# Kernel tuning notes

Measured on AMD Instinct MI355X. Metric: run time of the kernel, lower is better.

The kernel has to match this reference:

```python
import jax, jax.numpy as jnp
import numpy as np
from jax import lax

NCLASSES = 3
NMS_PRE = 100
NMS_THR = 0.01
SCORE_THR = 0.1
MAX_NUM = 50
H, W = 248, 216
BS = 16


def make_anchors():
    # Faithful to Anchors(ranges, sizes, rotations) in __init__.
    z0s = np.array([-0.6, -0.6, -1.78], np.float32)
    sizes = np.array([[0.6, 0.8, 1.73], [0.6, 1.76, 1.73], [1.6, 3.9, 1.56]], np.float32)
    rotations = np.array([0.0, 1.57], np.float32)
    x = (np.arange(W, dtype=np.float32) + 0.5) * (69.12 / W)
    y = (np.arange(H, dtype=np.float32) + 0.5) * (79.36 / H) - 39.68
    yy, xx = np.meshgrid(y, x, indexing='ij')  # (H, W)
    anchors = np.zeros((H, W, 3, 2, 7), np.float32)
    for c in range(3):
        for r in range(2):
            anchors[:, :, c, r, 0] = xx
            anchors[:, :, c, r, 1] = yy
            anchors[:, :, c, r, 2] = z0s[c]
            anchors[:, :, c, r, 3:6] = sizes[c]
            anchors[:, :, c, r, 6] = rotations[r]
    return jnp.asarray(anchors)


def setup_inputs() -> dict:
    key = jax.random.key(0)
    k1, k2, k3 = jax.random.split(key, 3)
    return {
        'bbox_cls_pred': jax.random.normal(k1, (BS, 18, H, W), jnp.float32),
        'bbox_pred': jax.random.normal(k2, (BS, 42, H, W), jnp.float32) * 0.1,
        'bbox_dir_cls_pred': jax.random.normal(k3, (BS, 12, H, W), jnp.float32),
        'anchors': make_anchors(),
    }


def limit_period(val, offset=1.0, period=np.pi):
    return val - jnp.floor(val / period + offset) * period


def anchors2bboxes(anchors, deltas):
    xa, ya, za, wa, la, ha, ra = [anchors[:, i] for i in range(7)]
    dx, dy, dz, dw, dl, dh, dr = [deltas[:, i] for i in range(7)]
    da = jnp.sqrt(wa * wa + la * la)
    x = dx * da + xa
    y = dy * da + ya
    z = dz * ha + za + ha * 0.5
    w = wa * jnp.exp(dw)
    l = la * jnp.exp(dl)
    h = ha * jnp.exp(dh)
    z = z - h * 0.5
    theta = ra + dr
    return jnp.stack([x, y, z, w, l, h, theta], axis=-1)


def nms_keep(boxes2d, scores, valid, thresh):
    # Greedy NMS over fixed NMS_PRE boxes; invalid boxes never kept / never suppress.
    n = scores.shape[0]
    order = jnp.argsort(-jnp.where(valid, scores, -jnp.inf))
    b = boxes2d[order]
    v = valid[order]
    area = (b[:, 2] - b[:, 0]) * (b[:, 3] - b[:, 1])
    x1 = jnp.maximum(b[:, None, 0], b[None, :, 0])
    y1 = jnp.maximum(b[:, None, 1], b[None, :, 1])
    x2 = jnp.minimum(b[:, None, 2], b[None, :, 2])
    y2 = jnp.minimum(b[:, None, 3], b[None, :, 3])
    inter = jnp.maximum(x2 - x1, 0.0) * jnp.maximum(y2 - y1, 0.0)
    iou = inter / (area[:, None] + area[None, :] - inter + 1e-8)
    idx = jnp.arange(n)
    def body(i, keep):
        sup = (iou[i] > thresh) & (idx > i) & keep[i]
        return keep & ~sup
    keep = lax.fori_loop(0, n, body, v)
    return jnp.zeros(n, bool).at[order].set(keep)


def process_single(cls_pred, box_pred, dir_pred, anchors):
    # cls_pred (18,H,W), box_pred (42,H,W), dir_pred (12,H,W), anchors (H,W,3,2,7)
    cls = jnp.transpose(cls_pred, (1, 2, 0)).reshape(-1, NCLASSES)
    box = jnp.transpose(box_pred, (1, 2, 0)).reshape(-1, 7)
    dirp = jnp.transpose(dir_pred, (1, 2, 0)).reshape(-1, 2)
    anc = anchors.reshape(-1, 7)
    cls = jax.nn.sigmoid(cls)
    dir_cls = jnp.argmax(dirp, axis=1)
    _, inds = lax.top_k(jnp.max(cls, axis=1), NMS_PRE)
    cls = cls[inds]
    box = box[inds]
    dir_cls = dir_cls[inds]
    anc = anc[inds]
    bboxes = anchors2bboxes(anc, box)  # (NMS_PRE, 7): x,y,z,w,l,h,theta
    xy = bboxes[:, :2]
    wl = bboxes[:, 3:5]
    boxes2d = jnp.concatenate([xy - wl / 2, xy + wl / 2], axis=-1)
    # Torch code detaches theta through limit_period; dir term is constant.
    theta = lax.stop_gradient(limit_period(bboxes[:, 6])) + (1.0 - dir_cls.astype(bboxes.dtype)) * np.pi
    bboxes = bboxes.at[:, 6].set(theta)
    keeps = []
    for c in range(NCLASSES):
        sc = cls[:, c]
        valid = sc > SCORE_THR
        keeps.append(nms_keep(boxes2d, sc, valid, NMS_THR) & valid)
    keep = jnp.stack(keeps)            # (3, NMS_PRE)
    scores_all = cls.T                 # (3, NMS_PRE)
    flat = jnp.where(keep, scores_all, -1.0).reshape(-1)
    final_scores, fi = lax.top_k(flat, MAX_NUM)
    sel = fi % NMS_PRE
    labels = fi // NMS_PRE
    out_bboxes = bboxes[sel]
    mask = final_scores > 0.0
    return out_bboxes, labels, final_scores, mask


def reference(bbox_cls_pred, bbox_pred, bbox_dir_cls_pred, anchors):
    f = jax.vmap(process_single, in_axes=(0, 0, 0, None))
    return f(bbox_cls_pred, bbox_pred, bbox_dir_cls_pred, anchors)
```

## Files before the change

### kernel.cpp

```cpp
#include <hip/hip_runtime.h>
#include <cstdint>

#pragma clang fp contract(off)

#define HH 248
#define WW 216
#define HW (HH*WW)
#define NROW (6*HW)
#define BATCH 16
#define NPRE 100
#define MAXNUM 50
#define NB 2048
#define CAP 2048
#define SBLK 53
#define K0 64
#define NSLOT (SBLK*K0)
#define QMAX 14
#define PIF 3.14159274101257324f

#define T0BKT 1966u

#define CNTB_OFF 0
#define KEYS_OFF 3584
#define SH_OFF   (KEYS_OFF + BATCH*SBLK*K0*8)

__device__ __forceinline__ float sigmoidf_ref(float x) {
    if (x >= 0.0f) {
        return 1.0f / (1.0f + expf(-x));
    } else {
        float e = expf(x);
        return e / (1.0f + e);
    }
}

__device__ __forceinline__ unsigned bucket_of(unsigned bits) {
    unsigned b = (bits >= 0x3F000000u) ? (1024u + ((bits - 0x3F000000u) >> 13))
                                       : (bits >> 20);
    return (b > (unsigned)(NB - 1)) ? (unsigned)(NB - 1) : b;
}

__device__ __forceinline__ void emit_one(unsigned bits, unsigned row,
                                         unsigned* hist, unsigned* lcnt,
                                         unsigned long long* kseg) {
    unsigned bk = bucket_of(bits);
    atomicAdd(&hist[bk], 1u);
    if (bk >= T0BKT) {
        unsigned pos = atomicAdd(lcnt, 1u);
        if (pos < (unsigned)K0)
            kseg[pos] = ((unsigned long long)bits << 32) |
                        (unsigned long long)(0xFFFFFFFFu - row);
    }
}

__global__ __launch_bounds__(256) void k_score(const float* __restrict__ cls,
                                               unsigned short* __restrict__ subhist,
                                               unsigned* __restrict__ cntB,
                                               unsigned long long* __restrict__ keys) {
    int t = threadIdx.x, blk = blockIdx.x, b = blockIdx.y;
    __shared__ unsigned hist[NB];
    __shared__ unsigned lcnt;
    for (int i = t; i < NB; i += 256) hist[i] = 0;
    if (t == 0) lcnt = 0;
    __syncthreads();

    unsigned long long* kseg = keys + (size_t)(b * SBLK + blk) * K0;
    int cell0 = blk * 1024 + t * 4;
    if (cell0 < HW) {
        const float* p = cls + (size_t)b * 18 * HW;
        #pragma unroll
        for (int a = 0; a < 6; ++a) {
            float4 l0 = *(const float4*)(p + (size_t)(a*3+0)*HW + cell0);
            float4 l1 = *(const float4*)(p + (size_t)(a*3+1)*HW + cell0);
            float4 l2 = *(const float4*)(p + (size_t)(a*3+2)*HW + cell0);
            unsigned b0 = __float_as_uint(sigmoidf_ref(fmaxf(l0.x, fmaxf(l1.x, l2.x))));
            unsigned b1 = __float_as_uint(sigmoidf_ref(fmaxf(l0.y, fmaxf(l1.y, l2.y))));
            unsigned b2 = __float_as_uint(sigmoidf_ref(fmaxf(l0.z, fmaxf(l1.z, l2.z))));
            unsigned b3 = __float_as_uint(sigmoidf_ref(fmaxf(l0.w, fmaxf(l1.w, l2.w))));
            emit_one(b0, (unsigned)((cell0+0)*6 + a), hist, &lcnt, kseg);
            emit_one(b1, (unsigned)((cell0+1)*6 + a), hist, &lcnt, kseg);
            emit_one(b2, (unsigned)((cell0+2)*6 + a), hist, &lcnt, kseg);
            emit_one(b3, (unsigned)((cell0+3)*6 + a), hist, &lcnt, kseg);
        }
    }
    __syncthreads();
    unsigned short* sh = subhist + (size_t)(b * SBLK + blk) * NB;
    for (int i = t; i < NB; i += 256) sh[i] = (unsigned short)hist[i];
    if (t == 0) cntB[b * SBLK + blk] = lcnt;
}

__global__ __launch_bounds__(256) void k_final(
    const float* __restrict__ cls, const float* __restrict__ box,
    const float* __restrict__ dir, const float* __restrict__ anc,
    const unsigned* __restrict__ cntB, const unsigned long long* __restrict__ keys,
    const unsigned short* __restrict__ subhist,
    float* __restrict__ out) {
    int b = blockIdx.x, t = threadIdx.x;

    __shared__ unsigned long long keyS[CAP];
    __shared__ int   selRow[NPRE];
    __shared__ float bb[NPRE][7];
    __shared__ float b2d[NPRE][4];
    __shared__ float areaS[NPRE];
    __shared__ float clsS[3][NPRE];
    __shared__ float svalS[3][NPRE];
    __shared__ int   ordS[3][NPRE];
    __shared__ int   rankS[3][NPRE];
    __shared__ float4 sbox[3][NPRE];
    __shared__ float  sarea[3][NPRE];
    __shared__ unsigned keepInit[3][4];
    __shared__ unsigned long long maskS[3][NPRE][2];
    __shared__ unsigned long long keepBits[3][2];
    __shared__ float flatS[3*NPRE];
    __shared__ unsigned hq[256];
    __shared__ unsigned wq[4];
    __shared__ unsigned cntS[SBLK];
    __shared__ int  tbS;
    __shared__ unsigned StbS;
    __shared__ int  safeS;
    __shared__ unsigned mcnt;

    if (t == 0) { tbS = -1; StbS = 0; mcnt = 0; }
    if (t < SBLK) cntS[t] = cntB[b * SBLK + t];
    __syncthreads();

    unsigned long long kq[QMAX];
    #pragma unroll
    for (int q = 0; q < QMAX; ++q) {
        unsigned long long kk = 0ULL;
        int s = t + q * 256;
        if (s < NSLOT) {
            int k = s >> 6, i = s & 63;
            if ((unsigned)i < cntS[k])
                kk = keys[(size_t)(b * SBLK + k) * K0 + i];
        }
        kq[q] = kk;
    }

    {
        const unsigned short* base = subhist + (size_t)b * SBLK * NB;
        unsigned carry = 0;
        for (int c0 = NB - 256; c0 >= 0; c0 -= 256) {
            unsigned s = 0;
            #pragma unroll 4
            for (int k = 0; k < SBLK; ++k) s += base[(size_t)k * NB + (c0 + t)];
            unsigned val = s;
            int lane = t & 63;
            #pragma unroll
            for (int d = 1; d < 64; d <<= 1) {
                unsigned y = __shfl_down(val, d, 64);
                if (lane + d < 64) val += y;
            }
            if (lane == 0) wq[t >> 6] = val;
            __syncthreads();
            unsigned tail = 0;
            for (int w2 = (t >> 6) + 1; w2 < 4; ++w2) tail += wq[w2];
            unsigned S = val + tail + carry;
            hq[t] = S;
            __syncthreads();
            unsigned Snext = (t < 255) ? hq[t + 1] : carry;
            if (S >= (unsigned)NPRE && Snext < (unsigned)NPRE) {
                tbS = c0 + t;
                StbS = S;
            }
            __syncthreads();
            if (tbS >= 0) break;
            carry = hq[0];
        }
    }
    int tb = (tbS < 0) ? 0 : tbS;

    if (t < 64) {
        unsigned c = (t < SBLK) ? cntS[t] : 0u;
        unsigned long long ov = __ballot(c > (unsigned)K0);
        if (t == 0)
            safeS = (tbS >= (int)T0BKT) && (ov == 0ULL) &&
                    (StbS <= (unsigned)CAP) ? 1 : 0;
    }
    __syncthreads();

    int M;
    if (safeS) {
        #pragma unroll
        for (int q = 0; q < QMAX; ++q) {
            unsigned long long kk = kq[q];
            if (bucket_of((unsigned)(kk >> 32)) >= (unsigned)tb) {
                unsigned pos = atomicAdd(&mcnt, 1u);
                keyS[pos] = kk;
            }
        }
        __syncthreads();
        M = (int)mcnt;
    } else {
        const float* p = cls + (size_t)b * 18 * HW;
        for (int cell = t; cell < HW; cell += 256) {
            for (int a = 0; a < 6; ++a) {
                float v0 = p[(size_t)(a*3+0)*HW + cell];
                float v1 = p[(size_t)(a*3+1)*HW + cell];
                float v2 = p[(size_t)(a*3+2)*HW + cell];
                unsigned bits = __float_as_uint(sigmoidf_ref(fmaxf(v0, fmaxf(v1, v2))));
                if (bucket_of(bits) >= (unsigned)tb) {
                    unsigned pos = atomicAdd(&mcnt, 1u);
                    if (pos < (unsigned)CAP)
                        keyS[pos] = ((unsigned long long)bits << 32) |
                                    (unsigned long long)(0xFFFFFFFFu - (unsigned)(cell*6 + a));
                }
            }
        }
        __syncthreads();
        M = (mcnt < (unsigned)CAP) ? (int)mcnt : CAP;
    }
    __syncthreads();

    for (int i = t; i < M; i += 256) {
        unsigned long long k = keyS[i];
        int r = 0;
        int j = 0;
        for (; j + 3 < M; j += 4) {
            unsigned long long a0 = keyS[j+0], a1 = keyS[j+1];
            unsigned long long a2 = keyS[j+2], a3 = keyS[j+3];
            r += (int)(a0 > k) + (int)(a1 > k) + (int)(a2 > k) + (int)(a3 > k);
        }
        for (; j < M; ++j) r += (int)(keyS[j] > k);
        if (r < NPRE) selRow[r] = (int)(0xFFFFFFFFu - (unsigned)(k & 0xFFFFFFFFull));
    }
    __syncthreads();

    if (t < NPRE) {
        int row = selRow[t];
        int a = row % 6;
        int cell = row / 6;
        const float* cb = cls + (size_t)b * 18 * HW + cell;
        clsS[0][t] = sigmoidf_ref(cb[(size_t)(a*3+0)*HW]);
        clsS[1][t] = sigmoidf_ref(cb[(size_t)(a*3+1)*HW]);
        clsS[2][t] = sigmoidf_ref(cb[(size_t)(a*3+2)*HW]);
        const float* db = dir + (size_t)b * 12 * HW + cell;
        float d0 = db[(size_t)(a*2+0)*HW];
        float d1 = db[(size_t)(a*2+1)*HW];
        int dircls = (d1 > d0) ? 1 : 0;
        const float* pb = box + (size_t)b * 42 * HW + cell;
        float dx = pb[(size_t)(a*7+0)*HW], dy = pb[(size_t)(a*7+1)*HW], dz = pb[(size_t)(a*7+2)*HW];
        float dw = pb[(size_t)(a*7+3)*HW], dl = pb[(size_t)(a*7+4)*HW], dh = pb[(size_t)(a*7+5)*HW];
        float dr = pb[(size_t)(a*7+6)*HW];
        const float* ab = anc + (size_t)row * 7;
        float xa = ab[0], ya = ab[1], za = ab[2];
        float wa = ab[3], la = ab[4], ha = ab[5], ra = ab[6];
        float da = sqrtf(wa*wa + la*la);
        float x = dx*da + xa;
        float y = dy*da + ya;
        float z = dz*ha + za + ha*0.5f;
        float wv = wa*expf(dw);
        float lv = la*expf(dl);
        float hv = ha*expf(dh);
        z = z - hv*0.5f;
        float th0 = ra + dr;
        float lim = th0 - floorf(th0/PIF + 1.0f)*PIF;
        float theta = lim + (1.0f - (float)dircls)*PIF;
        bb[t][0]=x; bb[t][1]=y; bb[t][2]=z; bb[t][3]=wv; bb[t][4]=lv; bb[t][5]=hv; bb[t][6]=theta;
        b2d[t][0] = x - wv*0.5f;
        b2d[t][1] = y - lv*0.5f;
        b2d[t][2] = x + wv*0.5f;
        b2d[t][3] = y + lv*0.5f;
        areaS[t] = (b2d[t][2]-b2d[t][0]) * (b2d[t][3]-b2d[t][1]);
    }
    if (t < 12) keepInit[t/4][t%4] = 0u;
    __syncthreads();

    for (int w = t; w < 3*NPRE; w += 256) {
        int c = w / NPRE, p = w % NPRE;
        float sc = clsS[c][p];
        svalS[c][p] = (sc > 0.1f) ? sc : -INFINITY;
    }
    __syncthreads();

    for (int w = t; w < 3*NPRE; w += 256) {
        int c = w / NPRE, p = w % NPRE;
        float v = svalS[c][p];
        int r = 0;
        for (int j0 = 0; j0 < NPRE; j0 += 4) {
            float v0 = svalS[c][j0+0], v1 = svalS[c][j0+1];
            float v2 = svalS[c][j0+2], v3 = svalS[c][j0+3];
            r += (int)(v0 > v || (v0 == v && (j0+0) < p));
            r += (int)(v1 > v || (v1 == v && (j0+1) < p));
            r += (int)(v2 > v || (v2 == v && (j0+2) < p));
            r += (int)(v3 > v || (v3 == v && (j0+3) < p));
        }
        ordS[c][r] = p;
        rankS[c][p] = r;
        if (v != -INFINITY) atomicOr(&keepInit[c][r >> 5], 1u << (r & 31));
    }
    __syncthreads();

    for (int w = t; w < 3*NPRE; w += 256) {
        int c = w / NPRE, i = w % NPRE;
        int pi = ordS[c][i];
        sbox[c][i] = make_float4(b2d[pi][0], b2d[pi][1], b2d[pi][2], b2d[pi][3]);
        sarea[c][i] = areaS[pi];
    }
    __syncthreads();

    for (int w = t; w < 3*NPRE; w += 256) {
        int c = w / NPRE, i = w % NPRE;
        float4 bi = sbox[c][i];
        float ai = sarea[c][i];
        unsigned long long m0 = 0ULL, m1 = 0ULL;
        #pragma unroll 2
        for (int j = i + 1; j < NPRE; ++j) {
            float4 bj = sbox[c][j];
            float x1 = fmaxf(bi.x, bj.x);
            float y1 = fmaxf(bi.y, bj.y);
            float x2 = fminf(bi.z, bj.z);
            float y2 = fminf(bi.w, bj.w);
            float inter = fmaxf(x2 - x1, 0.0f) * fmaxf(y2 - y1, 0.0f);
            float iou = inter / (ai + sarea[c][j] - inter + 1e-8f);
            unsigned long long hit = (iou > 0.01f) ? 1ULL : 0ULL;
            if (j < 64) m0 |= hit << j;
            else        m1 |= hit << (j - 64);
        }
        maskS[c][i][0] = m0;
        maskS[c][i][1] = m1;
    }
    __syncthreads();

    if (t < 3) {
        int c = t;
        unsigned long long k0 = (unsigned long long)keepInit[c][0] |
                                ((unsigned long long)keepInit[c][1] << 32);
        unsigned long long k1 = (unsigned long long)keepInit[c][2] |
                                ((unsigned long long)keepInit[c][3] << 32);
        unsigned long long todo = k0;
        while (todo) {
            int i = __builtin_ctzll(todo);
            unsigned long long m0 = maskS[c][i][0];
            unsigned long long m1 = maskS[c][i][1];
            k0 &= ~m0;
            k1 &= ~m1;
            todo = (todo & (todo - 1)) & ~m0;
        }
        todo = k1;
        while (todo) {
            int i = __builtin_ctzll(todo);
            unsigned long long m1 = maskS[c][64 + i][1];
            k1 &= ~m1;
            todo = (todo & (todo - 1)) & ~m1;
        }
        keepBits[c][0] = k0;
        keepBits[c][1] = k1;
    }
    __syncthreads();

    for (int w = t; w < 3*NPRE; w += 256) {
        int c = w / NPRE, p = w % NPRE;
        int r = rankS[c][p];
        unsigned long long bit = (r < 64) ? (keepBits[c][0] >> r) : (keepBits[c][1] >> (r - 64));
        flatS[w] = (bit & 1ULL) ? clsS[c][p] : -1.0f;
    }
    __syncthreads();

    for (int i = t; i < 3*NPRE; i += 256) {
        float vi = flatS[i];
        int r2 = 0;
        for (int j0 = 0; j0 < 3*NPRE; j0 += 4) {
            float v0 = flatS[j0+0], v1 = flatS[j0+1];
            float v2 = flatS[j0+2], v3 = flatS[j0+3];
            r2 += (int)(v0 > vi || (v0 == vi && (j0+0) < i));
            r2 += (int)(v1 > vi || (v1 == vi && (j0+1) < i));
            r2 += (int)(v2 > vi || (v2 == vi && (j0+2) < i));
            r2 += (int)(v3 > vi || (v3 == vi && (j0+3) < i));
        }
        if (r2 < MAXNUM) {
            int p = i % NPRE;
            int lab = i / NPRE;
            int o = b * MAXNUM + r2;
            float* ob = out + (size_t)o * 7;
            for (int j = 0; j < 7; ++j) ob[j] = bb[p][j];
            out[BATCH*MAXNUM*7 + o] = (float)lab;
            out[BATCH*MAXNUM*8 + o] = vi;
            out[BATCH*MAXNUM*9 + o] = (vi > 0.0f) ? 1.0f : 0.0f;
        }
    }
}

extern "C" void kernel_launch(void* const* d_in, const int* in_sizes, int n_in,
                              void* d_out, int out_size, void* d_ws, size_t ws_size,
                              hipStream_t stream) {
    const float* cls = (const float*)d_in[0];
    const float* box = (const float*)d_in[1];
    const float* dir = (const float*)d_in[2];
    const float* anc = (const float*)d_in[3];
    float* out = (float*)d_out;
    char* ws = (char*)d_ws;

    unsigned* cntB = (unsigned*)(ws + CNTB_OFF);
    unsigned long long* keys = (unsigned long long*)(ws + KEYS_OFF);
    unsigned short* subhist  = (unsigned short*)(ws + SH_OFF);

    dim3 g(SBLK, BATCH);
    k_score<<<g, 256, 0, stream>>>(cls, subhist, cntB, keys);
    k_final<<<BATCH, 256, 0, stream>>>(cls, box, dir, anc, cntB, keys, subhist, out);
}
```

Baseline: 297.8 us.

## Drop full score histogram; build threshold histogram from gathered candidate keys

The scoring kernel no longer keeps a 2048-bin shared histogram with an atomic per score, and no longer writes per-block sub-histograms to global memory. The final kernel now builds a small histogram over only the top buckets from the candidate keys it already loaded, then finds the top-100 threshold bucket with a suffix sum. When the fast path is not safe, a slow path rebuilds the full histogram from the raw scores. This removes the shared atomics, the sub-histogram global traffic and the 53-way reduction. The cost is that the fallback path becomes heavier.

```diff
diff --git a/kernel.cpp b/kernel.cpp
--- a/kernel.cpp
+++ b/kernel.cpp
@@ -19,10 +19,10 @@
 #define PIF 3.14159274101257324f
 
 #define T0BKT 1966u
+#define FBINS (NB - (int)T0BKT)
 
 #define CNTB_OFF 0
 #define KEYS_OFF 3584
-#define SH_OFF   (KEYS_OFF + BATCH*SBLK*K0*8)
 
 __device__ __forceinline__ float sigmoidf_ref(float x) {
     if (x >= 0.0f) {
@@ -40,11 +40,9 @@
 }
 
 __device__ __forceinline__ void emit_one(unsigned bits, unsigned row,
-                                         unsigned* hist, unsigned* lcnt,
+                                         unsigned* lcnt,
                                          unsigned long long* kseg) {
-    unsigned bk = bucket_of(bits);
-    atomicAdd(&hist[bk], 1u);
-    if (bk >= T0BKT) {
+    if (bucket_of(bits) >= T0BKT) {
         unsigned pos = atomicAdd(lcnt, 1u);
         if (pos < (unsigned)K0)
             kseg[pos] = ((unsigned long long)bits << 32) |
@@ -53,13 +51,10 @@
 }
 
 __global__ __launch_bounds__(256) void k_score(const float* __restrict__ cls,
-                                               unsigned short* __restrict__ subhist,
                                                unsigned* __restrict__ cntB,
                                                unsigned long long* __restrict__ keys) {
     int t = threadIdx.x, blk = blockIdx.x, b = blockIdx.y;
-    __shared__ unsigned hist[NB];
     __shared__ unsigned lcnt;
-    for (int i = t; i < NB; i += 256) hist[i] = 0;
     if (t == 0) lcnt = 0;
     __syncthreads();
 
@@ -76,15 +71,13 @@
             unsigned b1 = __float_as_uint(sigmoidf_ref(fmaxf(l0.y, fmaxf(l1.y, l2.y))));
             unsigned b2 = __float_as_uint(sigmoidf_ref(fmaxf(l0.z, fmaxf(l1.z, l2.z))));
             unsigned b3 = __float_as_uint(sigmoidf_ref(fmaxf(l0.w, fmaxf(l1.w, l2.w))));
-            emit_one(b0, (unsigned)((cell0+0)*6 + a), hist, &lcnt, kseg);
-            emit_one(b1, (unsigned)((cell0+1)*6 + a), hist, &lcnt, kseg);
-            emit_one(b2, (unsigned)((cell0+2)*6 + a), hist, &lcnt, kseg);
-            emit_one(b3, (unsigned)((cell0+3)*6 + a), hist, &lcnt, kseg);
-        }
-    }
-    __syncthreads();
-    unsigned short* sh = subhist + (size_t)(b * SBLK + blk) * NB;
-    for (int i = t; i < NB; i += 256) sh[i] = (unsigned short)hist[i];
+            emit_one(b0, (unsigned)((cell0+0)*6 + a), &lcnt, kseg);
+            emit_one(b1, (unsigned)((cell0+1)*6 + a), &lcnt, kseg);
+            emit_one(b2, (unsigned)((cell0+2)*6 + a), &lcnt, kseg);
+            emit_one(b3, (unsigned)((cell0+3)*6 + a), &lcnt, kseg);
+        }
+    }
+    __syncthreads();
     if (t == 0) cntB[b * SBLK + blk] = lcnt;
 }
 
@@ -92,7 +85,6 @@
     const float* __restrict__ cls, const float* __restrict__ box,
     const float* __restrict__ dir, const float* __restrict__ anc,
     const unsigned* __restrict__ cntB, const unsigned long long* __restrict__ keys,
-    const unsigned short* __restrict__ subhist,
     float* __restrict__ out) {
     int b = blockIdx.x, t = threadIdx.x;
 
@@ -111,15 +103,18 @@
     __shared__ unsigned long long maskS[3][NPRE][2];
     __shared__ unsigned long long keepBits[3][2];
     __shared__ float flatS[3*NPRE];
-    __shared__ unsigned hq[256];
-    __shared__ unsigned wq[4];
+    __shared__ unsigned fh[FBINS];
+    __shared__ unsigned fsuf[FBINS + 1];
     __shared__ unsigned cntS[SBLK];
+    __shared__ unsigned slowH[NB];
     __shared__ int  tbS;
     __shared__ unsigned StbS;
     __shared__ int  safeS;
     __shared__ unsigned mcnt;
 
     if (t == 0) { tbS = -1; StbS = 0; mcnt = 0; }
+    if (t < FBINS) fh[t] = 0;
+    if (t == FBINS) fsuf[FBINS] = 0;
     if (t < SBLK) cntS[t] = cntB[b * SBLK + t];
     __syncthreads();
 
@@ -136,48 +131,40 @@
         kq[q] = kk;
     }
 
-    {
-        const unsigned short* base = subhist + (size_t)b * SBLK * NB;
-        unsigned carry = 0;
-        for (int c0 = NB - 256; c0 >= 0; c0 -= 256) {
-            unsigned s = 0;
-            #pragma unroll 4
-            for (int k = 0; k < SBLK; ++k) s += base[(size_t)k * NB + (c0 + t)];
-            unsigned val = s;
-            int lane = t & 63;
-            #pragma unroll
-            for (int d = 1; d < 64; d <<= 1) {
-                unsigned y = __shfl_down(val, d, 64);
-                if (lane + d < 64) val += y;
-            }
-            if (lane == 0) wq[t >> 6] = val;
-            __syncthreads();
-            unsigned tail = 0;
-            for (int w2 = (t >> 6) + 1; w2 < 4; ++w2) tail += wq[w2];
-            unsigned S = val + tail + carry;
-            hq[t] = S;
-            __syncthreads();
-            unsigned Snext = (t < 255) ? hq[t + 1] : carry;
-            if (S >= (unsigned)NPRE && Snext < (unsigned)NPRE) {
-                tbS = c0 + t;
-                StbS = S;
-            }
-            __syncthreads();
-            if (tbS >= 0) break;
-            carry = hq[0];
-        }
-    }
-    int tb = (tbS < 0) ? 0 : tbS;
+    #pragma unroll
+    for (int q = 0; q < QMAX; ++q) {
+        unsigned bk = bucket_of((unsigned)(kq[q] >> 32));
+        if (bk >= T0BKT) atomicAdd(&fh[bk - T0BKT], 1u);
+    }
+    __syncthreads();
+
+    if (t < FBINS) {
+        unsigned s = 0;
+        int j = t;
+        for (; j + 3 < FBINS; j += 4)
+            s += fh[j] + fh[j+1] + fh[j+2] + fh[j+3];
+        for (; j < FBINS; ++j) s += fh[j];
+        fsuf[t] = s;
+    }
+    __syncthreads();
+    if (t < FBINS) {
+        unsigned S = fsuf[t], Sn = fsuf[t + 1];
+        if (S >= (unsigned)NPRE && Sn < (unsigned)NPRE) {
+            tbS = (int)T0BKT + t;
+            StbS = S;
+        }
+    }
+    __syncthreads();
 
     if (t < 64) {
         unsigned c = (t < SBLK) ? cntS[t] : 0u;
         unsigned long long ov = __ballot(c > (unsigned)K0);
         if (t == 0)
-            safeS = (tbS >= (int)T0BKT) && (ov == 0ULL) &&
-                    (StbS <= (unsigned)CAP) ? 1 : 0;
-    }
-    __syncthreads();
-
+            safeS = (tbS >= 0) && (ov == 0ULL) && (StbS <= (unsigned)CAP) ? 1 : 0;
+    }
+    __syncthreads();
+
+    int tb = tbS;
     int M;
     if (safeS) {
         #pragma unroll
@@ -191,7 +178,30 @@
         __syncthreads();
         M = (int)mcnt;
     } else {
+        for (int i = t; i < NB; i += 256) slowH[i] = 0;
+        __syncthreads();
         const float* p = cls + (size_t)b * 18 * HW;
+        for (int cell = t; cell < HW; cell += 256) {
+            for (int a = 0; a < 6; ++a) {
+                float v0 = p[(size_t)(a*3+0)*HW + cell];
+                float v1 = p[(size_t)(a*3+1)*HW + cell];
+                float v2 = p[(size_t)(a*3+2)*HW + cell];
+                unsigned bits = __float_as_uint(sigmoidf_ref(fmaxf(v0, fmaxf(v1, v2))));
+                atomicAdd(&slowH[bucket_of(bits)], 1u);
+            }
+        }
+        __syncthreads();
+        if (t == 0) {
+            unsigned cum = 0;
+            int r = 0;
+            for (int j = NB - 1; j >= 0; --j) {
+                cum += slowH[j];
+                if (cum >= (unsigned)NPRE) { r = j; break; }
+            }
+            tbS = r;
+        }
+        __syncthreads();
+        tb = tbS;
         for (int cell = t; cell < HW; cell += 256) {
             for (int a = 0; a < 6; ++a) {
                 float v0 = p[(size_t)(a*3+0)*HW + cell];
@@ -392,9 +402,8 @@
 
     unsigned* cntB = (unsigned*)(ws + CNTB_OFF);
     unsigned long long* keys = (unsigned long long*)(ws + KEYS_OFF);
-    unsigned short* subhist  = (unsigned short*)(ws + SH_OFF);
 
     dim3 g(SBLK, BATCH);
-    k_score<<<g, 256, 0, stream>>>(cls, subhist, cntB, keys);
-    k_final<<<BATCH, 256, 0, stream>>>(cls, box, dir, anc, cntB, keys, subhist, out);
-}
+    k_score<<<g, 256, 0, stream>>>(cls, cntB, keys);
+    k_final<<<BATCH, 256, 0, stream>>>(cls, box, dir, anc, cntB, keys, out);
+}
```

Measured after the change: 292.7 us. Within noise of the previous version (-1.7%).
